# Kernel optimization log

Hardware: AMD Instinct MI355X
Metric: run time of the kernel (lower is better)

## Reference

```python
import jax, jax.numpy as jnp
import numpy as np

NEG_BIG = -9e15


def gat_layer(h, adj, W, a, alpha, concat):
    # h: (N, Fin), W: (Fin, Fout), a: (2*Fout, 1)
    Wh = h @ W                                   # (N, Fout)
    F = Wh.shape[1]
    # e[i,j] = LeakyReLU(cat(Wh_i, Wh_j) @ a) = LeakyReLU(s_i + d_j)
    s = Wh @ a[:F, 0]                            # (N,)
    d = Wh @ a[F:, 0]                            # (N,)
    e = jax.nn.leaky_relu(s[:, None] + d[None, :], negative_slope=alpha)  # (N, N)
    e = jnp.where(adj > 0, e, NEG_BIG)
    att = jax.nn.softmax(e, axis=1)              # (N, N)
    out = att @ Wh                               # (N, Fout)
    return jax.nn.elu(out) if concat else out


def setup_inputs() -> dict:
    key = jax.random.key(0)
    ks = jax.random.split(key, 12)
    N, nfeat, nhid, nlatent, nclass = 8192, 512, 256, 64, 16

    def xavier(k, shape):
        gain = 1.414
        fan_in, fan_out = shape[0], shape[1]
        bound = gain * np.sqrt(6.0 / (fan_in + fan_out))
        return jax.random.uniform(k, shape, jnp.float32, -bound, bound)

    x = jax.random.normal(ks[0], (N, nfeat), jnp.float32)
    adj = jax.random.randint(ks[1], (N, N), 0, 2, jnp.int32)
    eps = jax.random.normal(ks[2], (N, nlatent), jnp.float32)
    return {
        "x": x,
        "adj": adj,
        "eps": eps,
        "W1": xavier(ks[3], (nfeat, nhid)),
        "a1": xavier(ks[4], (2 * nhid, 1)),
        "Wmu": xavier(ks[5], (nhid, nlatent)),
        "amu": xavier(ks[6], (2 * nlatent, 1)),
        "Wlv": xavier(ks[7], (nhid, nlatent)),
        "alv": xavier(ks[8], (2 * nlatent, 1)),
        "Wc": xavier(ks[9], (nlatent, nclass)),
        "bc": jnp.zeros((nclass,), jnp.float32),
    }


def reference(x, adj, eps, W1, a1, Wmu, amu, Wlv, alv, Wc, bc):
    alpha = 0.2  # LeakyReLU negative slope
    # eval mode: all dropouts are identity
    h = gat_layer(x, adj, W1, a1, alpha, concat=True)      # (N, nhid)
    mu = gat_layer(h, adj, Wmu, amu, alpha, concat=False)  # (N, nlatent)
    logvar = gat_layer(h, adj, Wlv, alv, alpha, concat=False)
    z = mu + eps * jnp.exp(0.5 * logvar)
    logits = z @ Wc + bc                                   # (N, nclass)
    return logits, mu, logvar
```

## Files before the change

### kernel.cpp

```cpp
#include <hip/hip_runtime.h>

typedef unsigned short u16;
typedef __attribute__((ext_vector_type(8))) short short8;
typedef __attribute__((ext_vector_type(4))) float f32x4;

#define NROW 8192

__device__ __forceinline__ float bf2f(u16 h) {
  unsigned u = ((unsigned)h) << 16;
  return __builtin_bit_cast(float, u);
}
__device__ __forceinline__ float ldf(const void* p, size_t i, int f32) {
  return f32 ? ((const float*)p)[i] : bf2f(((const u16*)p)[i]);
}
__device__ __forceinline__ u16 f2bf(float f) {
  unsigned b = __builtin_bit_cast(unsigned, f);
  b += 0x7FFFu + ((b >> 16) & 1u);
  return (u16)(b >> 16);
}

__global__ void detect3(const u16* __restrict__ xr, unsigned* __restrict__ mode) {
  __shared__ int zc, bg;
  int t = threadIdx.x;
  if (t == 0) { zc = 0; bg = 0; }
  __syncthreads();
  int zeros_even = 0; int big = 0;
  for (int i = t; i < 4096; i += 256) {
    u16 v = xr[i];
    if (!(i & 1) && v == 0) zeros_even++;
    if (fabsf(bf2f(v)) > 1e6f) big = 1;
  }
  atomicAdd(&zc, zeros_even);
  if (big) atomicOr(&bg, 1);
  __syncthreads();
  if (t == 0) *mode = (zc > 512 || bg) ? 1u : 0u;
}

__global__ void detect_adj(const unsigned* __restrict__ a, unsigned* __restrict__ amode) {
  __shared__ int clo;
  int t = threadIdx.x;
  if (t == 0) clo = 0;
  __syncthreads();
  int c = 0;
  for (int i = t; i < 4096; i += 256)
    if (a[i] == 0x00003F80u) c++;
  atomicAdd(&clo, c);
  __syncthreads();
  if (t == 0) *amode = (clo > 32) ? 1u : 0u;
}

__global__ __launch_bounds__(256) void adj_bits(const void* __restrict__ adj,
    unsigned char* __restrict__ bits, const unsigned* __restrict__ amodep) {
  int amode = (int)*amodep;
  for (size_t b = (size_t)blockIdx.x * 256 + threadIdx.x; b < 8388608; b += 524288) {
    size_t e0 = b * 8;
    unsigned byte = 0;
    if (amode == 0) {
      int4 a0 = *(const int4*)((const int*)adj + e0);
      int4 a1 = *(const int4*)((const int*)adj + e0 + 4);
      byte = (a0.x != 0) | ((a0.y != 0) << 1) | ((a0.z != 0) << 2) | ((a0.w != 0) << 3) |
             ((a1.x != 0) << 4) | ((a1.y != 0) << 5) | ((a1.z != 0) << 6) | ((a1.w != 0) << 7);
    } else {
      ushort4 a0 = *(const ushort4*)((const u16*)adj + e0);
      ushort4 a1 = *(const ushort4*)((const u16*)adj + e0 + 4);
      byte = (a0.x != 0) | ((a0.y != 0) << 1) | ((a0.z != 0) << 2) | ((a0.w != 0) << 3) |
             ((a1.x != 0) << 4) | ((a1.y != 0) << 5) | ((a1.z != 0) << 6) | ((a1.w != 0) << 7);
    }
    bits[b] = (unsigned char)byte;
  }
}

__global__ __launch_bounds__(256) void gemm_mfma(const u16* __restrict__ Abf,
    const u16* __restrict__ BT, float* __restrict__ C, int K, int N) {
  int tid = threadIdx.x;
  int l = tid & 63, w = tid >> 6;
  int m0 = blockIdx.y * 64, n0 = blockIdx.x * 64;
  const u16* arow = Abf + (size_t)(m0 + w * 16 + (l & 15)) * K + (l >> 4) * 8;
  const u16* brow = BT + (size_t)(n0 + (l & 15)) * K + (l >> 4) * 8;
  f32x4 acc[4];
#pragma unroll
  for (int nt = 0; nt < 4; ++nt) acc[nt] = (f32x4){0.f, 0.f, 0.f, 0.f};
  for (int k0 = 0; k0 < K; k0 += 32) {
    short8 a = *(const short8*)(arow + k0);
#pragma unroll
    for (int nt = 0; nt < 4; ++nt) {
      short8 b = *(const short8*)(brow + (size_t)nt * 16 * K + k0);
      acc[nt] = __builtin_amdgcn_mfma_f32_16x16x32_bf16(a, b, acc[nt], 0, 0, 0);
    }
  }
#pragma unroll
  for (int nt = 0; nt < 4; ++nt)
#pragma unroll
    for (int q = 0; q < 4; ++q)
      C[(size_t)(m0 + w * 16 + (l >> 4) * 4 + q) * N + n0 + nt * 16 + (l & 15)] =
          acc[nt][q];
}

__global__ __launch_bounds__(256) void gemm2_dual(const u16* __restrict__ Abf,
    const u16* __restrict__ BT0, const u16* __restrict__ BT1,
    float* __restrict__ C0, float* __restrict__ C1) {
  const int K = 256, N = 64;
  const u16* BT = blockIdx.x ? BT1 : BT0;
  float* C = blockIdx.x ? C1 : C0;
  int tid = threadIdx.x, l = tid & 63, w = tid >> 6;
  int m0 = blockIdx.y * 64;
  const u16* arow = Abf + (size_t)(m0 + w * 16 + (l & 15)) * K + (l >> 4) * 8;
  const u16* brow = BT + (size_t)(l & 15) * K + (l >> 4) * 8;
  f32x4 acc[4];
#pragma unroll
  for (int nt = 0; nt < 4; ++nt) acc[nt] = (f32x4){0.f, 0.f, 0.f, 0.f};
  for (int k0 = 0; k0 < K; k0 += 32) {
    short8 a = *(const short8*)(arow + k0);
#pragma unroll
    for (int nt = 0; nt < 4; ++nt) {
      short8 b = *(const short8*)(brow + (size_t)nt * 16 * K + k0);
      acc[nt] = __builtin_amdgcn_mfma_f32_16x16x32_bf16(a, b, acc[nt], 0, 0, 0);
    }
  }
#pragma unroll
  for (int nt = 0; nt < 4; ++nt)
#pragma unroll
    for (int q = 0; q < 4; ++q)
      C[(size_t)(m0 + w * 16 + (l >> 4) * 4 + q) * N + nt * 16 + (l & 15)] = acc[nt][q];
}

__global__ __launch_bounds__(256) void convert_bf16(const void* __restrict__ in,
    u16* __restrict__ out, int n8, const unsigned* __restrict__ modep) {
  int f32 = (int)*modep;
  int i = blockIdx.x * 256 + threadIdx.x;
  if (i >= n8) return;
  if (f32) {
    float4 v0 = ((const float4*)in)[(size_t)i * 2];
    float4 v1 = ((const float4*)in)[(size_t)i * 2 + 1];
    ushort4 o0 = {f2bf(v0.x), f2bf(v0.y), f2bf(v0.z), f2bf(v0.w)};
    ushort4 o1 = {f2bf(v1.x), f2bf(v1.y), f2bf(v1.z), f2bf(v1.w)};
    ((ushort4*)out)[(size_t)i * 2] = o0;
    ((ushort4*)out)[(size_t)i * 2 + 1] = o1;
  } else {
    ((int4*)out)[i] = ((const int4*)in)[i];
  }
}

__global__ __launch_bounds__(256) void transpose_bf16(const float* __restrict__ in,
    u16* __restrict__ out, int M, int F) {
  __shared__ float t[32][33];
  int m0 = blockIdx.x * 32, f0 = blockIdx.y * 32;
  int c = threadIdx.x & 31, r = threadIdx.x >> 5;
  for (int rr = r; rr < 32; rr += 8)
    t[rr][c] = in[(size_t)(m0 + rr) * F + f0 + c];
  __syncthreads();
  for (int rr = r; rr < 32; rr += 8)
    out[(size_t)(f0 + rr) * M + m0 + c] = f2bf(t[c][rr]);
}

__global__ __launch_bounds__(256) void transpose_pair(const float* __restrict__ in0,
    const float* __restrict__ in1, u16* __restrict__ out0, u16* __restrict__ out1,
    int M, int F) {
  const float* in = blockIdx.z ? in1 : in0;
  u16* out = blockIdx.z ? out1 : out0;
  __shared__ float t[32][33];
  int m0 = blockIdx.x * 32, f0 = blockIdx.y * 32;
  int c = threadIdx.x & 31, r = threadIdx.x >> 5;
  for (int rr = r; rr < 32; rr += 8)
    t[rr][c] = in[(size_t)(m0 + rr) * F + f0 + c];
  __syncthreads();
  for (int rr = r; rr < 32; rr += 8)
    out[(size_t)(f0 + rr) * M + m0 + c] = f2bf(t[c][rr]);
}

__global__ __launch_bounds__(256) void transpose_any(const void* __restrict__ in,
    u16* __restrict__ out, int M, int F, const unsigned* __restrict__ modep) {
  int f32 = (int)*modep;
  __shared__ u16 t[32][33];
  int m0 = blockIdx.x * 32, f0 = blockIdx.y * 32;
  int c = threadIdx.x & 31, r = threadIdx.x >> 5;
  for (int rr = r; rr < 32; rr += 8)
    t[rr][c] = f2bf(ldf(in, (size_t)(m0 + rr) * F + f0 + c, f32));
  __syncthreads();
  for (int rr = r; rr < 32; rr += 8)
    out[(size_t)(f0 + rr) * M + m0 + c] = t[c][rr];
}

__global__ __launch_bounds__(256) void transpose_w2(const void* __restrict__ in0,
    const void* __restrict__ in1, u16* __restrict__ out0, u16* __restrict__ out1,
    int M, int F, const unsigned* __restrict__ modep) {
  int f32 = (int)*modep;
  const void* in = blockIdx.z ? in1 : in0;
  u16* out = blockIdx.z ? out1 : out0;
  __shared__ u16 t[32][33];
  int m0 = blockIdx.x * 32, f0 = blockIdx.y * 32;
  int c = threadIdx.x & 31, r = threadIdx.x >> 5;
  for (int rr = r; rr < 32; rr += 8)
    t[rr][c] = f2bf(ldf(in, (size_t)(m0 + rr) * F + f0 + c, f32));
  __syncthreads();
  for (int rr = r; rr < 32; rr += 8)
    out[(size_t)(f0 + rr) * M + m0 + c] = t[c][rr];
}

__global__ __launch_bounds__(256) void sd_f32(const float* __restrict__ Wh,
    const void* __restrict__ a2, float* __restrict__ s, float* __restrict__ d,
    int F, const unsigned* __restrict__ modep) {
  int f32 = (int)*modep;
  int row = blockIdx.x * 4 + (threadIdx.x >> 6);
  int l = threadIdx.x & 63;
  float ss = 0.f, dd = 0.f;
  for (int k = l; k < F; k += 64) {
    float wv = Wh[(size_t)row * F + k];
    ss += wv * ldf(a2, k, f32);
    dd += wv * ldf(a2, F + k, f32);
  }
#pragma unroll
  for (int off = 32; off > 0; off >>= 1) {
    ss += __shfl_down(ss, off, 64);
    dd += __shfl_down(dd, off, 64);
  }
  if (l == 0) { s[row] = ss; d[row] = dd; }
}

__global__ __launch_bounds__(256) void sd_dual(const float* __restrict__ Wh0,
    const float* __restrict__ Wh1, const void* __restrict__ a0,
    const void* __restrict__ a1, float* __restrict__ s0, float* __restrict__ s1,
    float* __restrict__ d0, float* __restrict__ d1,
    const unsigned* __restrict__ modep) {
  int f32 = (int)*modep;
  int L = blockIdx.y;
  const float* Wh = L ? Wh1 : Wh0;
  const void* a2 = L ? a1 : a0;
  int row = blockIdx.x * 4 + (threadIdx.x >> 6);
  int l = threadIdx.x & 63;
  float wv = Wh[(size_t)row * 64 + l];
  float ss = wv * ldf(a2, l, f32);
  float dd = wv * ldf(a2, 64 + l, f32);
#pragma unroll
  for (int off = 32; off > 0; off >>= 1) {
    ss += __shfl_down(ss, off, 64);
    dd += __shfl_down(dd, off, 64);
  }
  if (l == 0) { (L ? s1 : s0)[row] = ss; (L ? d1 : d0)[row] = dd; }
}

__global__ __launch_bounds__(256) void dmax_reduce(const float* __restrict__ da,
    const float* __restrict__ db, float* __restrict__ cells) {
  const float* d = blockIdx.x ? db : da;
  __shared__ float red[256];
  float m = -3.4e38f;
  for (int i = threadIdx.x; i < NROW; i += 256) m = fmaxf(m, d[i]);
  red[threadIdx.x] = m;
  __syncthreads();
#pragma unroll
  for (int sft = 128; sft > 0; sft >>= 1) {
    if (threadIdx.x < sft) red[threadIdx.x] = fmaxf(red[threadIdx.x], red[threadIdx.x + sft]);
    __syncthreads();
  }
  if (threadIdx.x == 0) cells[blockIdx.x * 16] = red[0];
}

__device__ __forceinline__ int pa_off(int L, int ks, int mh, int row, int kg) {
  return ((L * 8 + ks * 2 + mh) << 10) + (row << 6) + ((kg ^ ((row >> 1) & 3)) << 4);
}

template <int NL>
__global__ __launch_bounds__(512, 2) void flash_mfma(
    const u16* __restrict__ whTa, const u16* __restrict__ whTb,
    const float* __restrict__ sa, const float* __restrict__ da,
    const float* __restrict__ sb, const float* __restrict__ db,
    const float* __restrict__ cella, const float* __restrict__ cellb,
    const unsigned char* __restrict__ abits,
    void* __restrict__ o0, void* __restrict__ o1,
    void* __restrict__ o2, void* __restrict__ o3) {
  constexpr int NIT = NROW / 128;
  constexpr int NTW = (NL == 1) ? 2 : 1;
  constexpr int FDIM = (NL == 1) ? 256 : 64;
  __shared__ __align__(16) char PA[2][NL * 8192];
  __shared__ __align__(16) float dd_[NL][NROW];
  __shared__ float sv_[NL][32], Ms_[NL][32], ls_[NL][32];
  int tid = threadIdx.x;
  int r0 = blockIdx.x * 32;
  if (tid < 32 * NL) {
    int L = tid >> 5, i = tid & 31;
    float Dm = L ? *cellb : *cella;
    float t0 = (L ? sb : sa)[r0 + i];
    sv_[L][i] = t0;
    float m = t0 + Dm;
    Ms_[L][i] = fmaxf(m, 0.2f * m);
  }
  for (int u = tid; u < NL * (NROW / 4); u += 512) {
    int L = u / (NROW / 4), uu = u - L * (NROW / 4);
    ((float4*)dd_[L])[uu] = ((const float4*)(L ? db : da))[uu];
  }
  __syncthreads();
  int sr = tid >> 4, sjo = tid & 15;
  int ks_w = sjo >> 2, kg_w = sjo & 3, mh_w = sr >> 4, row_w = sr & 15;
  int l = tid & 63, w = tid >> 6;
  int layer = (NL == 1) ? 0 : (w >> 2);
  int ntb = (NL == 1) ? (w * 2) : (w & 3);
  const u16* whT = layer ? whTb : whTa;
  f32x4 acc[2][NTW];
#pragma unroll
  for (int m = 0; m < 2; ++m)
#pragma unroll
    for (int n = 0; n < NTW; ++n) acc[m][n] = (f32x4){0.f, 0.f, 0.f, 0.f};
  float psum[NL];
#pragma unroll
  for (int L = 0; L < NL; ++L) psum[L] = 0.f;
  int bofs = (r0 + sr) * 1024 + sjo;

  unsigned char abA = abits[bofs];
  unsigned char abB = abits[bofs + 16];
  for (int it = 0; it < NIT; ++it) {
    int j0 = it * 128;
    int cur = it & 1;
    short8 bfr[4][NTW];
#pragma unroll
    for (int ks = 0; ks < 4; ++ks) {
      size_t jcol = (size_t)(j0 + ks * 32 + (l >> 4) * 8);
#pragma unroll
      for (int nt = 0; nt < NTW; ++nt)
        bfr[ks][nt] =
            *(const short8*)&whT[(size_t)((ntb + nt) * 16 + (l & 15)) * NROW + jcol];
    }
    unsigned char abN = abB;
    if (it + 2 < NIT) abN = abits[bofs + (it + 2) * 16];
    char* pab = PA[cur];
#pragma unroll
    for (int L = 0; L < NL; ++L) {
      float sv = sv_[L][sr], Mr = Ms_[L][sr];
      float4 dv0 = *(const float4*)&dd_[L][j0 + sjo * 8];
      float4 dv1 = *(const float4*)&dd_[L][j0 + sjo * 8 + 4];
      float dvv[8] = {dv0.x, dv0.y, dv0.z, dv0.w, dv1.x, dv1.y, dv1.z, dv1.w};
      short8 pk;
      float ps = 0.f;
#pragma unroll
      for (int q = 0; q < 8; ++q) {
        float t = sv + dvv[q];
        float e = fmaxf(t, 0.2f * t) - Mr;
        float p = ((abA >> q) & 1) ? __expf(e) : 0.f;
        ps += p;
        pk[q] = (short)f2bf(p);
      }
      psum[L] += ps;
      *(short8*)(pab + pa_off(L, ks_w, mh_w, row_w, kg_w)) = pk;
    }
    asm volatile("s_waitcnt lgkmcnt(0)" ::: "memory");
    __builtin_amdgcn_s_barrier();
    __builtin_amdgcn_sched_barrier(0);
    __builtin_amdgcn_s_setprio(1);
#pragma unroll
    for (int ks = 0; ks < 4; ++ks) {
      short8 a0 = *(const short8*)(pab + pa_off(layer, ks, 0, l & 15, l >> 4));
      short8 a1 = *(const short8*)(pab + pa_off(layer, ks, 1, l & 15, l >> 4));
#pragma unroll
      for (int nt = 0; nt < NTW; ++nt) {
        acc[0][nt] = __builtin_amdgcn_mfma_f32_16x16x32_bf16(a0, bfr[ks][nt],
                                                             acc[0][nt], 0, 0, 0);
        acc[1][nt] = __builtin_amdgcn_mfma_f32_16x16x32_bf16(a1, bfr[ks][nt],
                                                             acc[1][nt], 0, 0, 0);
      }
    }
    __builtin_amdgcn_s_setprio(0);
    abA = abB; abB = abN;
  }
  __syncthreads();
  float* red = (float*)PA;
#pragma unroll
  for (int L = 0; L < NL; ++L) red[L * 512 + tid] = psum[L];
  __syncthreads();
  if (tid < 32 * NL) {
    int L = tid >> 5, r = tid & 31;
    float t = 0.f;
#pragma unroll
    for (int q = 0; q < 16; ++q) t += red[L * 512 + r * 16 + q];
    ls_[L][r] = t;
  }
  __syncthreads();
  if constexpr (NL == 1) {
    u16* hb = (u16*)o0;
#pragma unroll
    for (int m = 0; m < 2; ++m)
#pragma unroll
      for (int nt = 0; nt < NTW; ++nt)
#pragma unroll
        for (int q = 0; q < 4; ++q) {
          int r = m * 16 + (l >> 4) * 4 + q;
          int c = (ntb + nt) * 16 + (l & 15);
          float x = acc[m][nt][q] / ls_[0][r];
          x = (x > 0.f) ? x : (__expf(x) - 1.f);
          hb[(size_t)(r0 + r) * FDIM + c] = f2bf(x);
        }
  } else {
    float* of = (float*)(layer ? o2 : o0);
    float* od = (float*)(layer ? o3 : o1);
#pragma unroll
    for (int m = 0; m < 2; ++m)
#pragma unroll
      for (int q = 0; q < 4; ++q) {
        int r = m * 16 + (l >> 4) * 4 + q;
        int c = ntb * 16 + (l & 15);
        float x = acc[m][0][q] / ls_[layer][r];
        size_t idx = (size_t)(r0 + r) * FDIM + c;
        of[idx] = x;
        od[idx] = x;
      }
  }
}

__global__ __launch_bounds__(256) void logits_f32(const float* __restrict__ mu,
    const float* __restrict__ lv, const void* __restrict__ eps,
    const void* __restrict__ Wc, const void* __restrict__ bcv,
    float* __restrict__ outL, const unsigned* __restrict__ modep) {
  int f32 = (int)*modep;
  __shared__ float zs[32 * 64];
  __shared__ float wcs[64 * 16];
  int tid = threadIdx.x;
  for (int i = tid; i < 1024; i += 256) wcs[i] = ldf(Wc, i, f32);
  int row0 = blockIdx.x * 32;
  for (int i = tid; i < 2048; i += 256) {
    int r = i >> 6, c = i & 63;
    size_t g = (size_t)(row0 + r) * 64 + c;
    zs[i] = mu[g] + ldf(eps, g, f32) * __expf(0.5f * lv[g]);
  }
  __syncthreads();
  for (int it = tid; it < 512; it += 256) {
    int r = it >> 4, oc = it & 15;
    float a = ldf(bcv, oc, f32);
    for (int c = 0; c < 64; ++c) a += zs[r * 64 + c] * wcs[c * 16 + oc];
    outL[(size_t)(row0 + r) * 16 + oc] = a;
  }
}

extern "C" void kernel_launch(void* const* d_in, const int* in_sizes, int n_in,
                              void* d_out, int out_size, void* d_ws, size_t ws_size,
                              hipStream_t stream) {
  (void)out_size; (void)ws_size;
  int ix = 0, iadj = 1, ieps = 2, iW1 = 3, ia1 = 4, iWmu = 5, iamu = 6,
      iWlv = 7, ialv = 8, iWc = 9, ibc = 10;
  {
    int fmu = -1, flv = -1, fam = -1, fal = -1;
    for (int i = 0; i < n_in; ++i) {
      switch (in_sizes[i]) {
        case 67108864: iadj = i; break;
        case 4194304:  ix   = i; break;
        case 524288:   ieps = i; break;
        case 131072:   iW1  = i; break;
        case 512:      ia1  = i; break;
        case 1024:     iWc  = i; break;
        case 16:       ibc  = i; break;
        case 16384:    if (fmu < 0) fmu = i; else flv = i; break;
        case 128:      if (fam < 0) fam = i; else fal = i; break;
        default: break;
      }
    }
    if (fmu >= 0 && flv >= 0) { iWmu = fmu; iWlv = flv; }
    if (fam >= 0 && fal >= 0) { iamu = fam; ialv = fal; }
  }
  const void* adj = d_in[iadj];
  char* ws = (char*)d_ws;
  const size_t KB = 1024, MB = 1024 * 1024;
  float* wh1   = (float*)(ws + 0);
  float* whmu  = (float*)(ws + 0);
  float* whlv  = (float*)(ws + 2 * MB);
  float* muf   = (float*)(ws + 4 * MB);
  float* lvf   = (float*)(ws + 6 * MB);
  u16*   xbf   = (u16*)(ws + 8 * MB);
  u16*   whT1  = (u16*)(ws + 8 * MB);
  u16*   hbf   = (u16*)(ws + 12 * MB);
  u16*   whmuT = (u16*)(ws + 20 * MB);
  u16*   whlvT = (u16*)(ws + 21 * MB);
  u16*   W1T   = (u16*)(ws + 22 * MB);
  u16*   WmuT  = (u16*)(ws + 22 * MB + 256 * KB);
  u16*   WlvT  = (u16*)(ws + 22 * MB + 288 * KB);
  float* s1    = (float*)(ws + 24 * MB + 96 * KB);
  float* d1    = (float*)(ws + 24 * MB + 128 * KB);
  float* smu   = (float*)(ws + 24 * MB + 160 * KB);
  float* dmu   = (float*)(ws + 24 * MB + 192 * KB);
  float* slv   = (float*)(ws + 24 * MB + 224 * KB);
  float* dlv   = (float*)(ws + 24 * MB + 256 * KB);
  float* dmaxv = (float*)(ws + 24 * MB + 288 * KB);
  unsigned* mode  = (unsigned*)(ws + 24 * MB + 289 * KB);
  unsigned* amode = (unsigned*)(ws + 24 * MB + 290 * KB);
  unsigned char* abits = (unsigned char*)(ws + 25 * MB);

  float* out_logits = (float*)d_out;
  float* out_mu     = (float*)d_out + 131072;
  float* out_lv     = (float*)d_out + 655360;

  detect3<<<1, 256, 0, stream>>>((const u16*)d_in[ix], mode);
  detect_adj<<<1, 256, 0, stream>>>((const unsigned*)adj, amode);
  adj_bits<<<2048, 256, 0, stream>>>(adj, abits, amode);

  convert_bf16<<<2048, 256, 0, stream>>>(d_in[ix], xbf, 524288, mode);
  transpose_any<<<dim3(16, 8), 256, 0, stream>>>(d_in[iW1], W1T, 512, 256, mode);
  gemm_mfma<<<dim3(4, 128), 256, 0, stream>>>(xbf, W1T, wh1, 512, 256);
  transpose_bf16<<<dim3(256, 8), 256, 0, stream>>>(wh1, whT1, 8192, 256);
  sd_f32<<<2048, 256, 0, stream>>>(wh1, d_in[ia1], s1, d1, 256, mode);
  dmax_reduce<<<1, 256, 0, stream>>>(d1, d1, dmaxv + 0);
  flash_mfma<1><<<256, 512, 0, stream>>>(whT1, nullptr, s1, d1,
      nullptr, nullptr, dmaxv + 0, nullptr, abits,
      hbf, nullptr, nullptr, nullptr);

  transpose_w2<<<dim3(8, 2, 2), 256, 0, stream>>>(d_in[iWmu], d_in[iWlv],
      WmuT, WlvT, 256, 64, mode);
  gemm2_dual<<<dim3(2, 128), 256, 0, stream>>>(hbf, WmuT, WlvT, whmu, whlv);
  transpose_pair<<<dim3(256, 2, 2), 256, 0, stream>>>(whmu, whlv, whmuT, whlvT,
      8192, 64);
  sd_dual<<<dim3(2048, 2), 256, 0, stream>>>(whmu, whlv, d_in[iamu], d_in[ialv],
      smu, slv, dmu, dlv, mode);
  dmax_reduce<<<2, 256, 0, stream>>>(dmu, dlv, dmaxv + 16);
  flash_mfma<2><<<256, 512, 0, stream>>>(whmuT, whlvT, smu, dmu, slv, dlv,
      dmaxv + 16, dmaxv + 32, abits,
      muf, out_mu, lvf, out_lv);

  logits_f32<<<256, 256, 0, stream>>>(muf, lvf, d_in[ieps], d_in[iWc], d_in[ibc], out_logits, mode);
}
```

Measured before the change: 736.5 us.

## Split attention K-dimension across waves and compute P fragments directly in registers

Rewrites the flash attention kernel so that each wave owns a slice of the neighbor (j) dimension and computes its own attention-probability A-fragments in registers. This removes the shared-memory staging of P and the per-iteration block barrier. Each wave now accumulates all output columns. Partial accumulators and row sums are reduced across waves through shared memory at the end. In exchange, register pressure rises with more accumulator tiles, the epilogue does a cross-wave reduction, and every wave reloads the full Wh^T B tiles for its slice.

```diff
diff --git a/kernel.cpp b/kernel.cpp
--- a/kernel.cpp
+++ b/kernel.cpp
@@ -153,21 +153,6 @@
     out[(size_t)(f0 + rr) * M + m0 + c] = f2bf(t[c][rr]);
 }
 
-__global__ __launch_bounds__(256) void transpose_pair(const float* __restrict__ in0,
-    const float* __restrict__ in1, u16* __restrict__ out0, u16* __restrict__ out1,
-    int M, int F) {
-  const float* in = blockIdx.z ? in1 : in0;
-  u16* out = blockIdx.z ? out1 : out0;
-  __shared__ float t[32][33];
-  int m0 = blockIdx.x * 32, f0 = blockIdx.y * 32;
-  int c = threadIdx.x & 31, r = threadIdx.x >> 5;
-  for (int rr = r; rr < 32; rr += 8)
-    t[rr][c] = in[(size_t)(m0 + rr) * F + f0 + c];
-  __syncthreads();
-  for (int rr = r; rr < 32; rr += 8)
-    out[(size_t)(f0 + rr) * M + m0 + c] = f2bf(t[c][rr]);
-}
-
 __global__ __launch_bounds__(256) void transpose_any(const void* __restrict__ in,
     u16* __restrict__ out, int M, int F, const unsigned* __restrict__ modep) {
   int f32 = (int)*modep;
@@ -195,6 +180,21 @@
   __syncthreads();
   for (int rr = r; rr < 32; rr += 8)
     out[(size_t)(f0 + rr) * M + m0 + c] = t[c][rr];
+}
+
+__global__ __launch_bounds__(256) void transpose_pair(const float* __restrict__ in0,
+    const float* __restrict__ in1, u16* __restrict__ out0, u16* __restrict__ out1,
+    int M, int F) {
+  const float* in = blockIdx.z ? in1 : in0;
+  u16* out = blockIdx.z ? out1 : out0;
+  __shared__ float t[32][33];
+  int m0 = blockIdx.x * 32, f0 = blockIdx.y * 32;
+  int c = threadIdx.x & 31, r = threadIdx.x >> 5;
+  for (int rr = r; rr < 32; rr += 8)
+    t[rr][c] = in[(size_t)(m0 + rr) * F + f0 + c];
+  __syncthreads();
+  for (int rr = r; rr < 32; rr += 8)
+    out[(size_t)(f0 + rr) * M + m0 + c] = f2bf(t[c][rr]);
 }
 
 __global__ __launch_bounds__(256) void sd_f32(const float* __restrict__ Wh,
@@ -255,12 +255,8 @@
   if (threadIdx.x == 0) cells[blockIdx.x * 16] = red[0];
 }
 
-__device__ __forceinline__ int pa_off(int L, int ks, int mh, int row, int kg) {
-  return ((L * 8 + ks * 2 + mh) << 10) + (row << 6) + ((kg ^ ((row >> 1) & 3)) << 4);
-}
-
 template <int NL>
-__global__ __launch_bounds__(512, 2) void flash_mfma(
+__global__ __launch_bounds__(512, 2) void flash_v2(
     const u16* __restrict__ whTa, const u16* __restrict__ whTb,
     const float* __restrict__ sa, const float* __restrict__ da,
     const float* __restrict__ sb, const float* __restrict__ db,
@@ -268,139 +264,136 @@
     const unsigned char* __restrict__ abits,
     void* __restrict__ o0, void* __restrict__ o1,
     void* __restrict__ o2, void* __restrict__ o3) {
-  constexpr int NIT = NROW / 128;
-  constexpr int NTW = (NL == 1) ? 2 : 1;
   constexpr int FDIM = (NL == 1) ? 256 : 64;
-  __shared__ __align__(16) char PA[2][NL * 8192];
+  constexpr int NT = FDIM / 16;
+  constexpr int NW_L = (NL == 1) ? 8 : 4;
+  constexpr int JSL = NROW / NW_L;
+  constexpr int NKS = JSL / 32;
   __shared__ __align__(16) float dd_[NL][NROW];
-  __shared__ float sv_[NL][32], Ms_[NL][32], ls_[NL][32];
-  int tid = threadIdx.x;
+  __shared__ float lsp[8][32];
+  __shared__ float ls_[NL][32];
+  int tid = threadIdx.x, l = tid & 63, w = tid >> 6;
   int r0 = blockIdx.x * 32;
-  if (tid < 32 * NL) {
-    int L = tid >> 5, i = tid & 31;
-    float Dm = L ? *cellb : *cella;
-    float t0 = (L ? sb : sa)[r0 + i];
-    sv_[L][i] = t0;
-    float m = t0 + Dm;
-    Ms_[L][i] = fmaxf(m, 0.2f * m);
-  }
+  int layer = (NL == 1) ? 0 : (w >> 2);
+  int wl = (NL == 1) ? w : (w & 3);
   for (int u = tid; u < NL * (NROW / 4); u += 512) {
     int L = u / (NROW / 4), uu = u - L * (NROW / 4);
     ((float4*)dd_[L])[uu] = ((const float4*)(L ? db : da))[uu];
   }
   __syncthreads();
-  int sr = tid >> 4, sjo = tid & 15;
-  int ks_w = sjo >> 2, kg_w = sjo & 3, mh_w = sr >> 4, row_w = sr & 15;
-  int l = tid & 63, w = tid >> 6;
-  int layer = (NL == 1) ? 0 : (w >> 2);
-  int ntb = (NL == 1) ? (w * 2) : (w & 3);
   const u16* whT = layer ? whTb : whTa;
-  f32x4 acc[2][NTW];
+  const float* sW = layer ? sb : sa;
+  const float* ddp = dd_[layer];
+  float Dm = layer ? *cellb : *cella;
+  int rlo = r0 + (l & 15);
+  float sv0 = sW[rlo], sv1 = sW[rlo + 16];
+  float t0 = sv0 + Dm, t1 = sv1 + Dm;
+  float Ms0 = fmaxf(t0, 0.2f * t0), Ms1 = fmaxf(t1, 0.2f * t1);
+  int jsbase = wl * JSL;
+  int koff = (l >> 4) * 8;
+  const uint4* pb0 = (const uint4*)(abits + (size_t)rlo * 1024 + (jsbase >> 3));
+  const uint4* pb1 = (const uint4*)(abits + (size_t)(rlo + 16) * 1024 + (jsbase >> 3));
+  f32x4 acc[2][NT];
 #pragma unroll
   for (int m = 0; m < 2; ++m)
 #pragma unroll
-    for (int n = 0; n < NTW; ++n) acc[m][n] = (f32x4){0.f, 0.f, 0.f, 0.f};
-  float psum[NL];
-#pragma unroll
-  for (int L = 0; L < NL; ++L) psum[L] = 0.f;
-  int bofs = (r0 + sr) * 1024 + sjo;
-
-  unsigned char abA = abits[bofs];
-  unsigned char abB = abits[bofs + 16];
-  for (int it = 0; it < NIT; ++it) {
-    int j0 = it * 128;
-    int cur = it & 1;
-    short8 bfr[4][NTW];
-#pragma unroll
-    for (int ks = 0; ks < 4; ++ks) {
-      size_t jcol = (size_t)(j0 + ks * 32 + (l >> 4) * 8);
-#pragma unroll
-      for (int nt = 0; nt < NTW; ++nt)
-        bfr[ks][nt] =
-            *(const short8*)&whT[(size_t)((ntb + nt) * 16 + (l & 15)) * NROW + jcol];
-    }
-    unsigned char abN = abB;
-    if (it + 2 < NIT) abN = abits[bofs + (it + 2) * 16];
-    char* pab = PA[cur];
-#pragma unroll
-    for (int L = 0; L < NL; ++L) {
-      float sv = sv_[L][sr], Mr = Ms_[L][sr];
-      float4 dv0 = *(const float4*)&dd_[L][j0 + sjo * 8];
-      float4 dv1 = *(const float4*)&dd_[L][j0 + sjo * 8 + 4];
+    for (int n = 0; n < NT; ++n) acc[m][n] = (f32x4){0.f, 0.f, 0.f, 0.f};
+  float psum0 = 0.f, psum1 = 0.f;
+  int bsh = (l >> 4) * 8;
+  uint4 aw0 = pb0[0], aw1 = pb1[0];
+  for (int g = 0; g < NKS / 4; ++g) {
+    uint4 c0 = aw0, c1 = aw1;
+    if (g + 1 < NKS / 4) { aw0 = pb0[g + 1]; aw1 = pb1[g + 1]; }
+    unsigned wd0[4] = {c0.x, c0.y, c0.z, c0.w};
+    unsigned wd1[4] = {c1.x, c1.y, c1.z, c1.w};
+#pragma unroll
+    for (int kk = 0; kk < 4; ++kk) {
+      int j0 = jsbase + (g * 4 + kk) * 32;
+      unsigned ab0 = (wd0[kk] >> bsh) & 0xffu;
+      unsigned ab1 = (wd1[kk] >> bsh) & 0xffu;
+      float4 dv0 = *(const float4*)&ddp[j0 + koff];
+      float4 dv1 = *(const float4*)&ddp[j0 + koff + 4];
       float dvv[8] = {dv0.x, dv0.y, dv0.z, dv0.w, dv1.x, dv1.y, dv1.z, dv1.w};
-      short8 pk;
-      float ps = 0.f;
+      short8 af0, af1;
 #pragma unroll
       for (int q = 0; q < 8; ++q) {
-        float t = sv + dvv[q];
-        float e = fmaxf(t, 0.2f * t) - Mr;
-        float p = ((abA >> q) & 1) ? __expf(e) : 0.f;
-        ps += p;
-        pk[q] = (short)f2bf(p);
+        float a0 = sv0 + dvv[q];
+        float e0 = fmaxf(a0, 0.2f * a0) - Ms0;
+        float p0 = ((ab0 >> q) & 1u) ? __expf(e0) : 0.f;
+        psum0 += p0;
+        af0[q] = (short)f2bf(p0);
+        float a1 = sv1 + dvv[q];
+        float e1 = fmaxf(a1, 0.2f * a1) - Ms1;
+        float p1 = ((ab1 >> q) & 1u) ? __expf(e1) : 0.f;
+        psum1 += p1;
+        af1[q] = (short)f2bf(p1);
       }
-      psum[L] += ps;
-      *(short8*)(pab + pa_off(L, ks_w, mh_w, row_w, kg_w)) = pk;
-    }
-    asm volatile("s_waitcnt lgkmcnt(0)" ::: "memory");
-    __builtin_amdgcn_s_barrier();
-    __builtin_amdgcn_sched_barrier(0);
-    __builtin_amdgcn_s_setprio(1);
-#pragma unroll
-    for (int ks = 0; ks < 4; ++ks) {
-      short8 a0 = *(const short8*)(pab + pa_off(layer, ks, 0, l & 15, l >> 4));
-      short8 a1 = *(const short8*)(pab + pa_off(layer, ks, 1, l & 15, l >> 4));
-#pragma unroll
-      for (int nt = 0; nt < NTW; ++nt) {
-        acc[0][nt] = __builtin_amdgcn_mfma_f32_16x16x32_bf16(a0, bfr[ks][nt],
-                                                             acc[0][nt], 0, 0, 0);
-        acc[1][nt] = __builtin_amdgcn_mfma_f32_16x16x32_bf16(a1, bfr[ks][nt],
-                                                             acc[1][nt], 0, 0, 0);
+      size_t jc = (size_t)(j0 + koff);
+#pragma unroll
+      for (int nt = 0; nt < NT; ++nt) {
+        short8 b = *(const short8*)&whT[(size_t)(nt * 16 + (l & 15)) * NROW + jc];
+        acc[0][nt] = __builtin_amdgcn_mfma_f32_16x16x32_bf16(af0, b, acc[0][nt], 0, 0, 0);
+        acc[1][nt] = __builtin_amdgcn_mfma_f32_16x16x32_bf16(af1, b, acc[1][nt], 0, 0, 0);
       }
     }
-    __builtin_amdgcn_s_setprio(0);
-    abA = abB; abB = abN;
-  }
-  __syncthreads();
-  float* red = (float*)PA;
-#pragma unroll
-  for (int L = 0; L < NL; ++L) red[L * 512 + tid] = psum[L];
+  }
+  psum0 += __shfl_xor(psum0, 16, 64); psum0 += __shfl_xor(psum0, 32, 64);
+  psum1 += __shfl_xor(psum1, 16, 64); psum1 += __shfl_xor(psum1, 32, 64);
+  if (l < 16) { lsp[w][l] = psum0; lsp[w][16 + l] = psum1; }
   __syncthreads();
   if (tid < 32 * NL) {
     int L = tid >> 5, r = tid & 31;
     float t = 0.f;
 #pragma unroll
-    for (int q = 0; q < 16; ++q) t += red[L * 512 + r * 16 + q];
+    for (int wv = 0; wv < NW_L; ++wv) t += lsp[L * NW_L + wv][r];
     ls_[L][r] = t;
   }
   __syncthreads();
+  float* red = (float*)dd_;
   if constexpr (NL == 1) {
     u16* hb = (u16*)o0;
 #pragma unroll
-    for (int m = 0; m < 2; ++m)
-#pragma unroll
-      for (int nt = 0; nt < NTW; ++nt)
-#pragma unroll
-        for (int q = 0; q < 4; ++q) {
-          int r = m * 16 + (l >> 4) * 4 + q;
-          int c = (ntb + nt) * 16 + (l & 15);
-          float x = acc[m][nt][q] / ls_[0][r];
-          x = (x > 0.f) ? x : (__expf(x) - 1.f);
-          hb[(size_t)(r0 + r) * FDIM + c] = f2bf(x);
-        }
+    for (int cg = 0; cg < 8; ++cg) {
+#pragma unroll
+      for (int mh = 0; mh < 2; ++mh)
+#pragma unroll
+        for (int ntl = 0; ntl < 2; ++ntl)
+#pragma unroll
+          for (int q = 0; q < 4; ++q)
+            red[w * 1024 + (mh * 16 + (l >> 4) * 4 + q) * 32 + ntl * 16 + (l & 15)] =
+                acc[mh][cg * 2 + ntl][q];
+      __syncthreads();
+      for (int e = tid; e < 1024; e += 512) {
+        int r = e >> 5, c = e & 31;
+        float x = 0.f;
+#pragma unroll
+        for (int wv = 0; wv < 8; ++wv) x += red[wv * 1024 + r * 32 + c];
+        x /= ls_[0][r];
+        x = (x > 0.f) ? x : (__expf(x) - 1.f);
+        hb[(size_t)(r0 + r) * 256 + cg * 32 + c] = f2bf(x);
+      }
+      __syncthreads();
+    }
   } else {
-    float* of = (float*)(layer ? o2 : o0);
-    float* od = (float*)(layer ? o3 : o1);
-#pragma unroll
-    for (int m = 0; m < 2; ++m)
-#pragma unroll
-      for (int q = 0; q < 4; ++q) {
-        int r = m * 16 + (l >> 4) * 4 + q;
-        int c = ntb * 16 + (l & 15);
-        float x = acc[m][0][q] / ls_[layer][r];
-        size_t idx = (size_t)(r0 + r) * FDIM + c;
-        of[idx] = x;
-        od[idx] = x;
-      }
+#pragma unroll
+    for (int mh = 0; mh < 2; ++mh)
+#pragma unroll
+      for (int nt = 0; nt < 4; ++nt)
+#pragma unroll
+        for (int q = 0; q < 4; ++q)
+          red[layer * 8192 + wl * 2048 + (mh * 16 + (l >> 4) * 4 + q) * 64 +
+              nt * 16 + (l & 15)] = acc[mh][nt][q];
+    __syncthreads();
+    for (int e = tid; e < 4096; e += 512) {
+      int L = e >> 11, rc = e & 2047, r = rc >> 6, c = rc & 63;
+      float x = 0.f;
+#pragma unroll
+      for (int wv = 0; wv < 4; ++wv) x += red[L * 8192 + wv * 2048 + r * 64 + c];
+      x /= ls_[L][r];
+      size_t gi = (size_t)(r0 + r) * 64 + c;
+      ((float*)(L ? o2 : o0))[gi] = x;
+      ((float*)(L ? o3 : o1))[gi] = x;
+    }
   }
 }
 
@@ -494,7 +487,7 @@
   transpose_bf16<<<dim3(256, 8), 256, 0, stream>>>(wh1, whT1, 8192, 256);
   sd_f32<<<2048, 256, 0, stream>>>(wh1, d_in[ia1], s1, d1, 256, mode);
   dmax_reduce<<<1, 256, 0, stream>>>(d1, d1, dmaxv + 0);
-  flash_mfma<1><<<256, 512, 0, stream>>>(whT1, nullptr, s1, d1,
+  flash_v2<1><<<256, 512, 0, stream>>>(whT1, nullptr, s1, d1,
       nullptr, nullptr, dmaxv + 0, nullptr, abits,
       hbf, nullptr, nullptr, nullptr);
 
@@ -506,7 +499,7 @@
   sd_dual<<<dim3(2048, 2), 256, 0, stream>>>(whmu, whlv, d_in[iamu], d_in[ialv],
       smu, slv, dmu, dlv, mode);
   dmax_reduce<<<2, 256, 0, stream>>>(dmu, dlv, dmaxv + 16);
-  flash_mfma<2><<<256, 512, 0, stream>>>(whmuT, whlvT, smu, dmu, slv, dlv,
+  flash_v2<2><<<256, 512, 0, stream>>>(whmuT, whlvT, smu, dmu, slv, dlv,
       dmaxv + 16, dmaxv + 32, abits,
       muf, out_mu, lvf, out_lv);
 
```

Result: slower. 757.2 us, median of 2 (+2.8%).
